# Performance work log

Hardware: AMD Instinct MI355X
Metric: run time of the kernel (lower is better)

Reference implementation:

```python
import jax, jax.numpy as jnp
import numpy as np

C_CURV = 1.0          # Poincare ball curvature c
EPS = 1e-15           # guard for norms / divisions
MAX_ATANH = 1.0 - 1e-5  # clamp artanh argument inside (-1, 1)


def _sqnorm(v):
    # squared norm along the manifold (channel) dim, axis=1
    return jnp.sum(v * v, axis=1, keepdims=True)


def _norm(v):
    return jnp.sqrt(jnp.clip(_sqnorm(v), EPS))


def _mobius_add(x, y, c):
    x2 = _sqnorm(x)
    y2 = _sqnorm(y)
    xy = jnp.sum(x * y, axis=1, keepdims=True)
    num = (1.0 + 2.0 * c * xy + c * y2) * x + (1.0 - c * x2) * y
    den = 1.0 + 2.0 * c * xy + (c * c) * x2 * y2
    return num / jnp.clip(den, EPS)


def _geodesic_midpoint(x, y, c):
    """expmap_x(0.5 * logmap_x(y)) on the Poincare ball, man_dim=1."""
    sc = jnp.sqrt(c)
    x2 = _sqnorm(x)
    lam = 2.0 / jnp.clip(1.0 - c * x2, EPS)  # conformal factor lambda_x
    # logmap_x(y)
    w = _mobius_add(-x, y, c)
    wn = _norm(w)
    v = (2.0 / (sc * lam)) * jnp.arctanh(jnp.clip(sc * wn, 0.0, MAX_ATANH)) * (w / wn)
    # half tangent vector
    v = 0.5 * v
    # expmap_x(v)
    vn = _norm(v)
    second = jnp.tanh(sc * lam * vn * 0.5) * (v / (sc * vn))
    return _mobius_add(x, second, c)


def setup_inputs() -> dict:
    key = jax.random.key(0)
    B, C, H, W = 8, 64, 128, 128
    n = jax.random.normal(key, (B, C, H, W), dtype=jnp.float32)
    # project strictly inside the unit ball along channel dim (valid Poincare points)
    nn_ = jnp.sqrt(jnp.clip(jnp.sum(n * n, axis=1, keepdims=True), EPS))
    x = 0.7 * n * jnp.tanh(nn_) / nn_
    return {"x": x}


def reference(x):
    c = C_CURV
    B, C_, H, W = x.shape
    Ho, Wo = 2 * H, 2 * W  # torch_like_size=True
    out = jnp.zeros((B, C_, Ho, Wo), dtype=x.dtype)
    # originals at even/even
    out = out.at[:, :, 0::2, 0::2].set(x)
    # horizontal midpoints: even rows, odd cols
    mid_h = _geodesic_midpoint(x[:, :, :, : W - 1], x[:, :, :, 1:], c)
    out = out.at[:, :, 0::2, 1:2 * (W - 1):2].set(mid_h)
    # vertical midpoints: odd rows, even cols
    mid_v = _geodesic_midpoint(x[:, :, : H - 1, :], x[:, :, 1:, :], c)
    out = out.at[:, :, 1:2 * (H - 1):2, 0::2].set(mid_v)
    # cell centers: bilinear via midpoints of horizontal midpoints
    x00 = x[:, :, : H - 1, : W - 1]
    x10 = x[:, :, : H - 1, 1:]
    x01 = x[:, :, 1:, : W - 1]
    x11 = x[:, :, 1:, 1:]
    a = _geodesic_midpoint(x00, x10, c)
    b = _geodesic_midpoint(x01, x11, c)
    center = _geodesic_midpoint(a, b, c)
    out = out.at[:, :, 1:2 * (H - 1):2, 1:2 * (W - 1):2].set(center)
    # torch-like size: duplicate last column/row
    out = out.at[:, :, :, -1].set(out[:, :, :, -2])
    out = out.at[:, :, -1, :].set(out[:, :, -2, :])
    return out
```

## Files before the change

kernel.cpp:

```cpp
#include <hip/hip_runtime.h>


#define EPSF   1e-15f
#define MAXAT  0.99999f

__device__ __forceinline__ void midcoef(float x2, float y2, float xy,
                                        float& A, float& B) {
    float alpha  = 1.0f - 2.0f * xy + y2;
    float beta   = 1.0f - x2;
    float den_w  = fmaxf(1.0f - 2.0f * xy + x2 * y2, EPSF);
    float inv_dw = 1.0f / den_w;
    float dxw = (beta * xy - alpha * x2) * inv_dw;
    float wn2 = (alpha * alpha * x2 - 2.0f * alpha * beta * xy + beta * beta * y2)
                * inv_dw * inv_dw;
    wn2 = fmaxf(wn2, EPSF);
    float wn = sqrtf(wn2);
    float a  = fminf(wn, MAXAT);
    float s  = a / (1.0f + sqrtf(fmaxf(1.0f - a * a, 0.0f)));
    float t  = s / wn;
    float xs = t * dxw;
    float s2 = t * t * wn2;
    float den     = fmaxf(1.0f + 2.0f * xs + x2 * s2, EPSF);
    float inv_den = 1.0f / den;
    float k = beta * t * inv_dw;
    A = (1.0f + 2.0f * xs + s2 - k * alpha * 0.0f) * inv_den - k * alpha * inv_den;
    A = ((1.0f + 2.0f * xs + s2) - k * alpha) * inv_den;
    B = (k * beta) * inv_den;
}

__global__ __launch_bounds__(128)
void hupsample_kernel(const float* __restrict__ x, float* __restrict__ out) {
    constexpr int B = 8, C = 64, H = 128, W = 128;
    constexpr int CS = H * W;
    const int w  = threadIdx.x;
    const int h  = blockIdx.x;
    const int b  = blockIdx.y;
    const int wp = (w + 1 < W) ? (w + 1) : (W - 1);
    const int hp = (h + 1 < H) ? (h + 1) : (H - 1);

    const float* xb  = x + (size_t)b * C * CS;
    const float* p00 = xb + h  * W + w;
    const float* p10 = xb + h  * W + wp;
    const float* p01 = xb + hp * W + w;
    const float* p11 = xb + hp * W + wp;

    float g00 = 0.f, g10 = 0.f, g01 = 0.f, g11 = 0.f;
    float d0010 = 0.f, d0111 = 0.f, d0001 = 0.f;
    float d0011 = 0.f, d1001 = 0.f, d1011 = 0.f;
#pragma unroll 4
    for (int c = 0; c < C; ++c) {
        float v00 = p00[c * CS];
        float v10 = p10[c * CS];
        float v01 = p01[c * CS];
        float v11 = p11[c * CS];
        g00   += v00 * v00;  g10   += v10 * v10;
        g01   += v01 * v01;  g11   += v11 * v11;
        d0010 += v00 * v10;  d0111 += v01 * v11;
        d0001 += v00 * v01;  d0011 += v00 * v11;
        d1001 += v10 * v01;  d1011 += v10 * v11;
    }

    float Ah, Bh;  midcoef(g00, g10, d0010, Ah, Bh);
    float A2, B2;  midcoef(g01, g11, d0111, A2, B2);
    float Av, Bv;  midcoef(g00, g01, d0001, Av, Bv);

    float a2 = Ah * Ah * g00 + 2.0f * Ah * Bh * d0010 + Bh * Bh * g10;
    float b2 = A2 * A2 * g01 + 2.0f * A2 * B2 * d0111 + B2 * B2 * g11;
    float ab = Ah * A2 * d0001 + Ah * B2 * d0011 + Bh * A2 * d1001 + Bh * B2 * d1011;
    float A3, B3;  midcoef(a2, b2, ab, A3, B3);
    float CA = A3 * Ah, CB = A3 * Bh, CC = B3 * A2, CD = B3 * B2;

    float* ob = out + (size_t)b * C * (2 * H) * (2 * W);
    const size_t rbase = (size_t)(2 * h) * (2 * W) + (size_t)(2 * w);
#pragma unroll 4
    for (int c = 0; c < C; ++c) {
        float v00 = p00[c * CS];
        float v10 = p10[c * CS];
        float v01 = p01[c * CS];
        float v11 = p11[c * CS];
        float oh = Ah * v00 + Bh * v10;
        float ov = Av * v00 + Bv * v01;
        float oc = CA * v00 + CB * v10 + CC * v01 + CD * v11;
        size_t base = (size_t)c * (4 * CS) + rbase;
        *(float2*)(ob + base)             = make_float2(v00, oh);
        *(float2*)(ob + base + 2 * W)     = make_float2(ov, oc);
    }
}

extern "C" void kernel_launch(void* const* d_in, const int* in_sizes, int n_in,
                              void* d_out, int out_size, void* d_ws, size_t ws_size,
                              hipStream_t stream) {
    const float* x = (const float*)d_in[0];
    float* out = (float*)d_out;
    dim3 grid(128, 8);
    dim3 block(128);
    hipLaunchKernelGGL(hupsample_kernel, grid, block, 0, stream, x, out);
}
```

Baseline: 167.0 us.

## Split channel reduction across four thread rows with shared-memory combine

```diff
diff --git a/kernel.cpp b/kernel.cpp
--- a/kernel.cpp
+++ b/kernel.cpp
@@ -23,22 +23,27 @@
     float den     = fmaxf(1.0f + 2.0f * xs + x2 * s2, EPSF);
     float inv_den = 1.0f / den;
     float k = beta * t * inv_dw;
-    A = (1.0f + 2.0f * xs + s2 - k * alpha * 0.0f) * inv_den - k * alpha * inv_den;
     A = ((1.0f + 2.0f * xs + s2) - k * alpha) * inv_den;
     B = (k * beta) * inv_den;
 }
 
-__global__ __launch_bounds__(128)
+__global__ __launch_bounds__(512)
 void hupsample_kernel(const float* __restrict__ x, float* __restrict__ out) {
-    constexpr int B = 8, C = 64, H = 128, W = 128;
+    constexpr int C = 64, H = 128, W = 128;
     constexpr int CS = H * W;
+    constexpr int CPS = C / 4;
+
+    __shared__ float part[4][128][11];
+    __shared__ float coef[128][9];
+
     const int w  = threadIdx.x;
+    const int s  = threadIdx.y;
     const int h  = blockIdx.x;
     const int b  = blockIdx.y;
     const int wp = (w + 1 < W) ? (w + 1) : (W - 1);
     const int hp = (h + 1 < H) ? (h + 1) : (H - 1);
 
-    const float* xb  = x + (size_t)b * C * CS;
+    const float* xb  = x + (size_t)b * C * CS + (size_t)(s * CPS) * CS;
     const float* p00 = xb + h  * W + w;
     const float* p10 = xb + h  * W + wp;
     const float* p01 = xb + hp * W + w;
@@ -48,7 +53,7 @@
     float d0010 = 0.f, d0111 = 0.f, d0001 = 0.f;
     float d0011 = 0.f, d1001 = 0.f, d1011 = 0.f;
 #pragma unroll 4
-    for (int c = 0; c < C; ++c) {
+    for (int c = 0; c < CPS; ++c) {
         float v00 = p00[c * CS];
         float v10 = p10[c * CS];
         float v01 = p01[c * CS];
@@ -59,21 +64,48 @@
         d0001 += v00 * v01;  d0011 += v00 * v11;
         d1001 += v10 * v01;  d1011 += v10 * v11;
     }
+    part[s][w][0] = g00;   part[s][w][1] = g10;
+    part[s][w][2] = g01;   part[s][w][3] = g11;
+    part[s][w][4] = d0010; part[s][w][5] = d0111;
+    part[s][w][6] = d0001; part[s][w][7] = d0011;
+    part[s][w][8] = d1001; part[s][w][9] = d1011;
+    __syncthreads();
 
-    float Ah, Bh;  midcoef(g00, g10, d0010, Ah, Bh);
-    float A2, B2;  midcoef(g01, g11, d0111, A2, B2);
-    float Av, Bv;  midcoef(g00, g01, d0001, Av, Bv);
+    if (s == 0) {
+        float t0[10];
+#pragma unroll
+        for (int k = 0; k < 10; ++k)
+            t0[k] = part[0][w][k] + part[1][w][k] + part[2][w][k] + part[3][w][k];
+        float G00 = t0[0], G10 = t0[1], G01 = t0[2], G11 = t0[3];
+        float D0010 = t0[4], D0111 = t0[5], D0001 = t0[6];
+        float D0011 = t0[7], D1001 = t0[8], D1011 = t0[9];
 
-    float a2 = Ah * Ah * g00 + 2.0f * Ah * Bh * d0010 + Bh * Bh * g10;
-    float b2 = A2 * A2 * g01 + 2.0f * A2 * B2 * d0111 + B2 * B2 * g11;
-    float ab = Ah * A2 * d0001 + Ah * B2 * d0011 + Bh * A2 * d1001 + Bh * B2 * d1011;
-    float A3, B3;  midcoef(a2, b2, ab, A3, B3);
-    float CA = A3 * Ah, CB = A3 * Bh, CC = B3 * A2, CD = B3 * B2;
+        float Ah, Bh;  midcoef(G00, G10, D0010, Ah, Bh);
+        float A2, B2;  midcoef(G01, G11, D0111, A2, B2);
+        float Av, Bv;  midcoef(G00, G01, D0001, Av, Bv);
 
-    float* ob = out + (size_t)b * C * (2 * H) * (2 * W);
+        float a2 = Ah * Ah * G00 + 2.0f * Ah * Bh * D0010 + Bh * Bh * G10;
+        float b2 = A2 * A2 * G01 + 2.0f * A2 * B2 * D0111 + B2 * B2 * G11;
+        float ab = Ah * A2 * D0001 + Ah * B2 * D0011
+                 + Bh * A2 * D1001 + Bh * B2 * D1011;
+        float A3, B3;  midcoef(a2, b2, ab, A3, B3);
+
+        coef[w][0] = Ah;      coef[w][1] = Bh;
+        coef[w][2] = Av;      coef[w][3] = Bv;
+        coef[w][4] = A3 * Ah; coef[w][5] = A3 * Bh;
+        coef[w][6] = B3 * A2; coef[w][7] = B3 * B2;
+    }
+    __syncthreads();
+
+    const float Ah = coef[w][0], Bh = coef[w][1];
+    const float Av = coef[w][2], Bv = coef[w][3];
+    const float CA = coef[w][4], CB = coef[w][5];
+    const float CC = coef[w][6], CD = coef[w][7];
+
+    float* ob = out + (size_t)b * C * (4 * CS) + (size_t)(s * CPS) * (4 * CS);
     const size_t rbase = (size_t)(2 * h) * (2 * W) + (size_t)(2 * w);
 #pragma unroll 4
-    for (int c = 0; c < C; ++c) {
+    for (int c = 0; c < CPS; ++c) {
         float v00 = p00[c * CS];
         float v10 = p10[c * CS];
         float v01 = p01[c * CS];
@@ -82,8 +114,8 @@
         float ov = Av * v00 + Bv * v01;
         float oc = CA * v00 + CB * v10 + CC * v01 + CD * v11;
         size_t base = (size_t)c * (4 * CS) + rbase;
-        *(float2*)(ob + base)             = make_float2(v00, oh);
-        *(float2*)(ob + base + 2 * W)     = make_float2(ov, oc);
+        *(float2*)(ob + base)         = make_float2(v00, oh);
+        *(float2*)(ob + base + 2 * W) = make_float2(ov, oc);
     }
 }
 
@@ -93,6 +125,6 @@
     const float* x = (const float*)d_in[0];
     float* out = (float*)d_out;
     dim3 grid(128, 8);
-    dim3 block(128);
+    dim3 block(128, 4);
     hipLaunchKernelGGL(hupsample_kernel, grid, block, 0, stream, x, out);
 }
```

New measurement: 168.3 us. About the same (+0.8%).
